# Performance work log

Hardware: AMD Instinct MI355X
Metric: run time of the kernel (lower is better)

Reference implementation:

```python
import jax, jax.numpy as jnp
import numpy as np

N = 100000   # nodes
DEG = 32     # in-degree per node
E = N * DEG  # 3.2M edges
D = 24       # node feature dim
NK = 2       # number of anisotropic kernels (tile(...,2) in source forces 2)
H = 64       # MLP hidden/out channels


def setup_inputs() -> dict:
    key = jax.random.key(0)
    k1, k2, k3, k4 = jax.random.split(key, 4)
    x = jax.random.normal(k1, (N, D), dtype=jnp.float32)
    src = jax.random.randint(k2, (E,), 0, N)
    tgt = jnp.repeat(jnp.arange(N), DEG)  # every node has DEG in-edges -> no 0/0
    edge_index = jnp.stack([src, tgt]).astype(jnp.int64)
    kvals = jax.random.normal(k3, (NK, E), dtype=jnp.float32)
    # Linear(2*D -> H, bias=False), xavier-like scale
    W = jax.random.normal(k4, (H, NK * D), dtype=jnp.float32) * (1.0 / (NK * D))
    return {"x": x, "edge_index": edge_index, "kvals": kvals, "W": W}


def reference(x, edge_index, kvals, W):
    src, tgt = edge_index[0], edge_index[1]
    xs = x[src]  # [E, D] gathered source features
    # per-kernel sparse aggregation: out_k[i] = sum_{e: tgt[e]==i} kvals[k,e] * x[src[e]]
    out = jnp.concatenate(
        [jax.ops.segment_sum(kvals[k][:, None] * xs, tgt, num_segments=N)
         for k in range(NK)], axis=1)  # [N, NK*D]
    # adj_norm: subtract tiled neighbor mean
    deg = jax.ops.segment_sum(jnp.ones((E,), x.dtype), tgt, num_segments=N)  # [N]
    sum_x = jax.ops.segment_sum(xs, tgt, num_segments=N)  # [N, D]
    norm_x = sum_x / deg[:, None]
    out = out - jnp.tile(norm_x, (1, NK)) + jnp.tile(x, (1, NK))
    # MLP: single bias-free linear, no activation
    return out @ W.T  # [N, H]
```

## Files before the change

kernel.cpp:

```cpp
#include <hip/hip_runtime.h>


#define NN   100000
#define DEG  32
#define EE   (NN * DEG)
#define DD   24
#define HH   64
#define NPB  32
#define TPB  256
#define NPW  8
#define PST  56
#define XRU  32

typedef __attribute__((ext_vector_type(8)))  short short8;
typedef __attribute__((ext_vector_type(16))) float float16;
typedef __attribute__((ext_vector_type(4)))  float f32x4;
typedef __attribute__((ext_vector_type(4)))  int   i32x4;
typedef __attribute__((ext_vector_type(4)))  unsigned short u16x4;

__device__ __forceinline__ unsigned short f2bf(float f) {
    union { float f; unsigned u; } v; v.f = f;
    unsigned r = v.u + 0x7fffu + ((v.u >> 16) & 1u);
    return (unsigned short)(r >> 16);
}

__device__ __forceinline__ float bf2f(unsigned u) {
    union { unsigned i; float f; } v; v.i = u << 16; return v.f;
}

__device__ __forceinline__ unsigned pk(unsigned a, unsigned b) {
    return __builtin_amdgcn_perm(b, a, 0x05040100u);
}

__device__ __forceinline__ short8 mk8(unsigned u0, unsigned u1, unsigned u2, unsigned u3) {
    union { unsigned u[4]; short8 s; } p;
    p.u[0] = u0; p.u[1] = u1; p.u[2] = u2; p.u[3] = u3;
    return p.s;
}

__global__ void xcvt(const float* __restrict__ x, unsigned short* __restrict__ xb, int n6) {
    int c = blockIdx.x * blockDim.x + threadIdx.x;
    if (c < n6) {
        int row = c / 6;
        int pos = c - row * 6;
        f32x4 v = __builtin_nontemporal_load(((const f32x4*)x) + c);
        u16x4 o;
        o.x = f2bf(v.x); o.y = f2bf(v.y); o.z = f2bf(v.z); o.w = f2bf(v.w);
        ((u16x4*)xb)[row * 8 + pos] = o;
    }
}

__global__ __launch_bounds__(TPB, 4) void gnn(
    const unsigned short* __restrict__ xb,
    const int*            __restrict__ ei,
    const float*          __restrict__ kv,
    const float*          __restrict__ W,
    float*                __restrict__ out)
{
    __shared__ int            ei_s[NPB * DEG];
    __shared__ unsigned short kv_s[2 * NPB * DEG];
    __shared__ unsigned short pre_s[NPB * PST];
    __shared__ unsigned short xs_s[4][64 * XRU];

    const int t    = threadIdx.x;
    const int lane = t & 63;
    const int w    = t >> 6;
    const int m    = lane & 31;
    const int kh   = lane >> 5;
    const int kh8  = kh * 8;
    const int base = blockIdx.x * NPB;
    const int dclamp = (m < DD) ? m : (DD - 1);
    const int m2     = dclamp * 2;
    const char* xbc  = (const char*)xb;

    const int er   = lane >> 2;
    const int q16  = (lane & 3) * 16;
    char* xsb = (char*)&xs_s[w][0];
    const unsigned wswz = (unsigned)((lane & 32) << 1);
    const unsigned fswz = (unsigned)(kh << 6);

    {
        const size_t eb = (size_t)base * DEG;
        i32x4 ev = __builtin_nontemporal_load(((const i32x4*)(ei + eb)) + t);
        ev.x <<= 6; ev.y <<= 6; ev.z <<= 6; ev.w <<= 6;
        ((i32x4*)ei_s)[t] = ev;
        const f32x4 c0 = __builtin_nontemporal_load(((const f32x4*)(kv + eb)) + t);
        const f32x4 c1 = __builtin_nontemporal_load(((const f32x4*)(kv + EE + eb)) + t);
        u16x4 u0, u1;
        u0.x = f2bf(c0.x); u0.y = f2bf(c0.y); u0.z = f2bf(c0.z); u0.w = f2bf(c0.w);
        u1.x = f2bf(c1.x); u1.y = f2bf(c1.y); u1.z = f2bf(c1.z); u1.w = f2bf(c1.w);
        ((u16x4*)kv_s)[t] = u0;
        ((u16x4*)(kv_s + NPB * DEG))[t] = u1;
    }
    __syncthreads();

    const unsigned short* kvrow = kv_s + (m & 1) * (NPB * DEG);

    i32x4 G[2][4];
    unsigned short xvv[2][2];

    #define GATHER_GANG(gg, sl) do {                                           \
        const int eb_ = (w * NPW + 2 * (gg)) * DEG;                            \
        const int o0_ = ei_s[eb_ +  0 + er];                                   \
        const int o1_ = ei_s[eb_ + 16 + er];                                   \
        const int o2_ = ei_s[eb_ + 32 + er];                                   \
        const int o3_ = ei_s[eb_ + 48 + er];                                   \
        G[sl][0] = *(const i32x4*)(xbc + (unsigned)(o0_ + q16));               \
        G[sl][1] = *(const i32x4*)(xbc + (unsigned)(o1_ + q16));               \
        G[sl][2] = *(const i32x4*)(xbc + (unsigned)(o2_ + q16));               \
        G[sl][3] = *(const i32x4*)(xbc + (unsigned)(o3_ + q16));               \
        xvv[sl][0] = xb[(base + w * NPW + 2 * (gg)) * XRU + dclamp];           \
        xvv[sl][1] = xb[(base + w * NPW + 2 * (gg) + 1) * XRU + dclamp];       \
    } while (0)

    #define WRITE_GANG(sl) do {                                                \
        *(i32x4*)(xsb + (((0 * 1024) + er * 64 + q16) ^ wswz)) = G[sl][0];     \
        *(i32x4*)(xsb + (((1 * 1024) + er * 64 + q16) ^ wswz)) = G[sl][1];     \
        *(i32x4*)(xsb + (((2 * 1024) + er * 64 + q16) ^ wswz)) = G[sl][2];     \
        *(i32x4*)(xsb + (((3 * 1024) + er * 64 + q16) ^ wswz)) = G[sl][3];     \
    } while (0)

    #define COMPUTE_NODE(nn, gg, sl) do {                                      \
        const int nl_ = w * NPW + 2 * (gg) + (nn);                             \
        const char* fb_ = xsb + (nn) * 2048 + (kh << 9);                       \
        unsigned ga_[8], gb_[8];                                               \
        _Pragma("unroll")                                                      \
        for (int j = 0; j < 8; ++j)                                            \
            ga_[j] = *(const unsigned short*)(fb_ + (((j << 6) + m2) ^ fswz)); \
        _Pragma("unroll")                                                      \
        for (int j = 0; j < 8; ++j)                                            \
            gb_[j] = *(const unsigned short*)(fb_ + 1024 + (((j << 6) + m2) ^ fswz)); \
        const int el_ = nl_ * DEG + kh8;                                       \
        const short8 raw0_ = *(const short8*)(kvrow + el_);                    \
        const short8 raw1_ = *(const short8*)(kvrow + el_ + 16);               \
        const unsigned fill_ = (m == 2) ? 0x3F803F80u : 0u;                    \
        const short8 af0_ = (m < 2) ? raw0_ : mk8(fill_, fill_, fill_, fill_); \
        const short8 af1_ = (m < 2) ? raw1_ : mk8(fill_, fill_, fill_, fill_); \
        const short8 bf0_ = mk8(pk(ga_[0], ga_[1]), pk(ga_[2], ga_[3]),        \
                                pk(ga_[4], ga_[5]), pk(ga_[6], ga_[7]));       \
        const short8 bf1_ = mk8(pk(gb_[0], gb_[1]), pk(gb_[2], gb_[3]),        \
                                pk(gb_[4], gb_[5]), pk(gb_[6], gb_[7]));       \
        float16 acc_;                                                          \
        _Pragma("unroll")                                                      \
        for (int r = 0; r < 16; ++r) acc_[r] = 0.f;                            \
        acc_ = __builtin_amdgcn_mfma_f32_32x32x16_bf16(af0_, bf0_, acc_, 0, 0, 0); \
        acc_ = __builtin_amdgcn_mfma_f32_32x32x16_bf16(af1_, bf1_, acc_, 0, 0, 0); \
        if (kh == 0 && m < DD) {                                               \
            const float sm_ = acc_[2] * (1.f / 32.f);                          \
            const float pv_ = bf2f(xvv[sl][nn]) - sm_;                         \
            pre_s[nl_ * PST + m]      = f2bf(acc_[0] + pv_);                   \
            pre_s[nl_ * PST + 24 + m] = f2bf(acc_[1] + pv_);                   \
        }                                                                      \
    } while (0)

    GATHER_GANG(0, 0);

    #pragma unroll
    for (int gg = 0; gg < NPW / 2; ++gg) {
        const int sl = gg & 1;
        WRITE_GANG(sl);
        if (gg < NPW / 2 - 1) GATHER_GANG(gg + 1, sl ^ 1);
        COMPUTE_NODE(0, gg, sl);
        COMPUTE_NODE(1, gg, sl);
    }
    #undef GATHER_GANG
    #undef WRITE_GANG
    #undef COMPUTE_NODE
    __syncthreads();

    if (w < 2) {
        const int h = w * 32 + m;

        float16 acc;
        #pragma unroll
        for (int r = 0; r < 16; ++r) acc[r] = 0.f;

        #pragma unroll
        for (int kc = 0; kc < 3; ++kc) {
            const int c0 = kc * 16 + kh8;
            const short8 af = *(const short8*)(pre_s + m * PST + c0);
            const float* wr = W + h * 48 + c0;
            const f32x4 wA = ((const f32x4*)wr)[0];
            const f32x4 wB = ((const f32x4*)wr)[1];
            const short8 bf = mk8(pk(f2bf(wA.x), f2bf(wA.y)), pk(f2bf(wA.z), f2bf(wA.w)),
                                  pk(f2bf(wB.x), f2bf(wB.y)), pk(f2bf(wB.z), f2bf(wB.w)));
            acc = __builtin_amdgcn_mfma_f32_32x32x16_bf16(af, bf, acc, 0, 0, 0);
        }

        #pragma unroll
        for (int r = 0; r < 16; ++r) {
            const int row = (r & 3) + 8 * (r >> 2) + 4 * kh;
            __builtin_nontemporal_store(acc[r], &out[(size_t)(base + row) * HH + h]);
        }
    }
}

extern "C" void kernel_launch(void* const* d_in, const int* in_sizes, int n_in,
                              void* d_out, int out_size, void* d_ws, size_t ws_size,
                              hipStream_t stream) {
    const float* x  = (const float*)d_in[0];
    const int*   ei = (const int*)d_in[1];
    const float* kv = (const float*)d_in[2];
    const float* W  = (const float*)d_in[3];
    float* out = (float*)d_out;

    unsigned short* xb = (unsigned short*)d_ws;
    const int n6 = NN * 6;
    xcvt<<<(n6 + 255) / 256, 256, 0, stream>>>(x, xb, n6);

    const int grid = NN / NPB;
    gnn<<<grid, TPB, 0, stream>>>(xb, ei, kv, W, out);
}
```

Measured before the change: 129.1 us.

## Issue all neighbor gathers up front and zero-fill padded bf16 rows

The main kernel now issues all four gang gathers (16 vector loads per lane) and the eight self-feature loads before any compute, instead of double-buffering one gang ahead. This puts more memory requests in flight per wave to hide gather latency, at the cost of more vector registers, which may cut occupancy at the 4-blocks-per-SM launch bound. The conversion kernel also writes the full 32-element padded row with zeros in the pad and uses shifts instead of a divide by six, so the padding lanes hold defined values.

```diff
diff --git a/kernel.cpp b/kernel.cpp
--- a/kernel.cpp
+++ b/kernel.cpp
@@ -38,15 +38,17 @@
     return p.s;
 }
 
-__global__ void xcvt(const float* __restrict__ x, unsigned short* __restrict__ xb, int n6) {
+__global__ void xcvt(const float* __restrict__ x, unsigned short* __restrict__ xb, int n8) {
     int c = blockIdx.x * blockDim.x + threadIdx.x;
-    if (c < n6) {
-        int row = c / 6;
-        int pos = c - row * 6;
-        f32x4 v = __builtin_nontemporal_load(((const f32x4*)x) + c);
-        u16x4 o;
-        o.x = f2bf(v.x); o.y = f2bf(v.y); o.z = f2bf(v.z); o.w = f2bf(v.w);
-        ((u16x4*)xb)[row * 8 + pos] = o;
+    if (c < n8) {
+        const int row = c >> 3;
+        const int pos = c & 7;
+        u16x4 o = (u16x4){0, 0, 0, 0};
+        if (pos < 6) {
+            f32x4 v = __builtin_nontemporal_load(((const f32x4*)x) + row * 6 + pos);
+            o.x = f2bf(v.x); o.y = f2bf(v.y); o.z = f2bf(v.z); o.w = f2bf(v.w);
+        }
+        ((u16x4*)xb)[c] = o;
     }
 }
 
@@ -96,31 +98,29 @@
 
     const unsigned short* kvrow = kv_s + (m & 1) * (NPB * DEG);
 
-    i32x4 G[2][4];
-    unsigned short xvv[2][2];
-
-    #define GATHER_GANG(gg, sl) do {                                           \
+    i32x4 G[4][4];
+    unsigned xv8[NPW];
+
+    #define GATHER_GANG(gg) do {                                               \
         const int eb_ = (w * NPW + 2 * (gg)) * DEG;                            \
         const int o0_ = ei_s[eb_ +  0 + er];                                   \
         const int o1_ = ei_s[eb_ + 16 + er];                                   \
         const int o2_ = ei_s[eb_ + 32 + er];                                   \
         const int o3_ = ei_s[eb_ + 48 + er];                                   \
-        G[sl][0] = *(const i32x4*)(xbc + (unsigned)(o0_ + q16));               \
-        G[sl][1] = *(const i32x4*)(xbc + (unsigned)(o1_ + q16));               \
-        G[sl][2] = *(const i32x4*)(xbc + (unsigned)(o2_ + q16));               \
-        G[sl][3] = *(const i32x4*)(xbc + (unsigned)(o3_ + q16));               \
-        xvv[sl][0] = xb[(base + w * NPW + 2 * (gg)) * XRU + dclamp];           \
-        xvv[sl][1] = xb[(base + w * NPW + 2 * (gg) + 1) * XRU + dclamp];       \
+        G[gg][0] = *(const i32x4*)(xbc + (unsigned)(o0_ + q16));               \
+        G[gg][1] = *(const i32x4*)(xbc + (unsigned)(o1_ + q16));               \
+        G[gg][2] = *(const i32x4*)(xbc + (unsigned)(o2_ + q16));               \
+        G[gg][3] = *(const i32x4*)(xbc + (unsigned)(o3_ + q16));               \
     } while (0)
 
-    #define WRITE_GANG(sl) do {                                                \
-        *(i32x4*)(xsb + (((0 * 1024) + er * 64 + q16) ^ wswz)) = G[sl][0];     \
-        *(i32x4*)(xsb + (((1 * 1024) + er * 64 + q16) ^ wswz)) = G[sl][1];     \
-        *(i32x4*)(xsb + (((2 * 1024) + er * 64 + q16) ^ wswz)) = G[sl][2];     \
-        *(i32x4*)(xsb + (((3 * 1024) + er * 64 + q16) ^ wswz)) = G[sl][3];     \
+    #define WRITE_GANG(gg) do {                                                \
+        *(i32x4*)(xsb + (((0 * 1024) + er * 64 + q16) ^ wswz)) = G[gg][0];     \
+        *(i32x4*)(xsb + (((1 * 1024) + er * 64 + q16) ^ wswz)) = G[gg][1];     \
+        *(i32x4*)(xsb + (((2 * 1024) + er * 64 + q16) ^ wswz)) = G[gg][2];     \
+        *(i32x4*)(xsb + (((3 * 1024) + er * 64 + q16) ^ wswz)) = G[gg][3];     \
     } while (0)
 
-    #define COMPUTE_NODE(nn, gg, sl) do {                                      \
+    #define COMPUTE_NODE(nn, gg) do {                                          \
         const int nl_ = w * NPW + 2 * (gg) + (nn);                             \
         const char* fb_ = xsb + (nn) * 2048 + (kh << 9);                       \
         unsigned ga_[8], gb_[8];                                               \
@@ -147,21 +147,26 @@
         acc_ = __builtin_amdgcn_mfma_f32_32x32x16_bf16(af1_, bf1_, acc_, 0, 0, 0); \
         if (kh == 0 && m < DD) {                                               \
             const float sm_ = acc_[2] * (1.f / 32.f);                          \
-            const float pv_ = bf2f(xvv[sl][nn]) - sm_;                         \
+            const float pv_ = bf2f(xv8[2 * (gg) + (nn)]) - sm_;                \
             pre_s[nl_ * PST + m]      = f2bf(acc_[0] + pv_);                   \
             pre_s[nl_ * PST + 24 + m] = f2bf(acc_[1] + pv_);                   \
         }                                                                      \
     } while (0)
 
-    GATHER_GANG(0, 0);
+    #pragma unroll
+    for (int nn = 0; nn < NPW; ++nn)
+        xv8[nn] = xb[(size_t)(base + w * NPW + nn) * XRU + dclamp];
+
+    GATHER_GANG(0);
+    GATHER_GANG(1);
+    GATHER_GANG(2);
+    GATHER_GANG(3);
 
     #pragma unroll
     for (int gg = 0; gg < NPW / 2; ++gg) {
-        const int sl = gg & 1;
-        WRITE_GANG(sl);
-        if (gg < NPW / 2 - 1) GATHER_GANG(gg + 1, sl ^ 1);
-        COMPUTE_NODE(0, gg, sl);
-        COMPUTE_NODE(1, gg, sl);
+        WRITE_GANG(gg);
+        COMPUTE_NODE(0, gg);
+        COMPUTE_NODE(1, gg);
     }
     #undef GATHER_GANG
     #undef WRITE_GANG
@@ -205,8 +210,8 @@
     float* out = (float*)d_out;
 
     unsigned short* xb = (unsigned short*)d_ws;
-    const int n6 = NN * 6;
-    xcvt<<<(n6 + 255) / 256, 256, 0, stream>>>(x, xb, n6);
+    const int n8 = NN * 8;
+    xcvt<<<(n8 + 255) / 256, 256, 0, stream>>>(x, xb, n8);
 
     const int grid = NN / NPB;
     gnn<<<grid, TPB, 0, stream>>>(xb, ei, kv, W, out);
```

Measured after the change: 130.6 us. Within noise of the previous version (+1.1%).
